# Kernel optimization log

Measured on AMD Instinct MI355X. Metric: run time of the kernel, lower is better.

## Reference

```python
import jax, jax.numpy as jnp
import numpy as np

B, T, N, D = 16, 48, 256, 64
K_HEADS = 8


def setup_inputs() -> dict:
    key = jax.random.key(0)
    ks = jax.random.split(key, 12)
    return {
        "query": jax.random.normal(ks[0], (B, T, N, D), jnp.float32),
        "key": jax.random.normal(ks[1], (B, T, N, D), jnp.float32),
        "value": jax.random.normal(ks[2], (B, T, N, D), jnp.float32),
        "key_w": jax.random.normal(ks[3], (B, T, D, D), jnp.float32) * 0.05,
        "key_b": jax.random.normal(ks[4], (B, T, D), jnp.float32) * 0.05,
        "value_w": jax.random.normal(ks[5], (B, T, D, D), jnp.float32) * 0.05,
        "value_b": jax.random.normal(ks[6], (B, T, D), jnp.float32) * 0.05,
        "proj1_w": jax.random.normal(ks[7], (D, D), jnp.float32) * 0.05,
        "proj1_b": jax.random.normal(ks[8], (D,), jnp.float32) * 0.05,
        "proj2_w": jax.random.normal(ks[9], (D, D), jnp.float32) * 0.05,
        "proj2_b": jax.random.normal(ks[10], (D,), jnp.float32) * 0.05,
        "rate": jnp.full((1,), 0.8, jnp.float32),
    }


def reference(query, key, value, key_w, key_b, value_w, value_b,
              proj1_w, proj1_b, proj2_w, proj2_b, rate):
    b, t, n, d = query.shape
    hs = d // K_HEADS
    # per-(batch,time) projections (LinearCustom)
    k = jnp.einsum('btnd,btde->btne', key, key_w) + key_b[:, :, None, :]
    v = jnp.einsum('btnd,btde->btne', value, value_w) + value_b[:, :, None, :]
    # split heads along channel dim (matches torch.split on dim -1)
    qh = query.reshape(b, t, n, K_HEADS, hs)
    kh = k.reshape(b, t, n, K_HEADS, hs)
    vh = v.reshape(b, t, n, K_HEADS, hs)
    # scores: [b, h, n, q, k]
    scores = jnp.einsum('bqnhd,bknhd->bhnqk', qh, kh) / jnp.sqrt(jnp.asarray(hs, query.dtype))
    # time decay: b_time_decays[..., i, j] = (T-1-i) + 1 = T - i (depends on query pos only)
    dec = (t - jnp.arange(t, dtype=scores.dtype))[:, None]  # [T, 1], broadcasts over key axis
    s = jax.nn.sigmoid(scores)
    denom = 1.0 + jax.nn.sigmoid(s * jax.nn.sigmoid(rate) * dec)
    att = jax.nn.softmax(jnp.tanh(s / denom), axis=-1)
    x = jnp.einsum('bhnqk,bknhd->bqnhd', att, vh).reshape(b, t, n, d)
    x = jnp.tanh(x @ proj1_w.T + proj1_b)
    return x @ proj2_w.T + proj2_b
```

## Files before the change

### kernel.cpp

```cpp
#include <hip/hip_runtime.h>


#define B_ 16
#define T_ 48
#define N_ 256
#define D_ 64

__device__ __forceinline__ float rcpf(float x) { return __builtin_amdgcn_rcpf(x); }
__device__ __forceinline__ float ex2(float x) { return __builtin_amdgcn_exp2f(x); }
#define LOG2E 1.4426950408889634f

__global__ __launch_bounds__(256) void proj_kv_kernel(
    const float* __restrict__ key, const float* __restrict__ key_w, const float* __restrict__ key_b,
    const float* __restrict__ value, const float* __restrict__ value_w, const float* __restrict__ value_b,
    float* __restrict__ k_out, float* __restrict__ v_out)
{
    const int bt = blockIdx.x;
    const int which = blockIdx.y;
    const float* __restrict__ in = (which ? value : key) + (size_t)bt * N_ * D_;
    const float* __restrict__ w  = (which ? value_w : key_w) + (size_t)bt * D_ * D_;
    const float* __restrict__ bb = (which ? value_b : key_b) + (size_t)bt * D_;
    float* __restrict__ out = (which ? v_out : k_out) + (size_t)bt * N_ * D_;

    __shared__ float Wl[D_][D_];
    __shared__ float Xl[128][68];
    __shared__ float Bl[D_];

    const int tid = threadIdx.x;
    #pragma unroll
    for (int i = tid; i < D_ * D_; i += 256) Wl[i >> 6][i & 63] = w[i];
    if (tid < D_) Bl[tid] = bb[tid];

    const int cg = tid & 7;
    const int rg = tid >> 3;

    for (int n0 = 0; n0 < N_; n0 += 128) {
        __syncthreads();
        #pragma unroll
        for (int i = tid; i < 128 * D_ / 4; i += 256) {
            const int e = i * 4;
            *(float4*)&Xl[e >> 6][e & 63] = *(const float4*)&in[(size_t)n0 * D_ + e];
        }
        __syncthreads();

        float acc[4][8];
        #pragma unroll
        for (int j = 0; j < 4; ++j)
            #pragma unroll
            for (int i = 0; i < 8; ++i) acc[j][i] = Bl[cg * 8 + i];

        #pragma unroll 8
        for (int d = 0; d < D_; ++d) {
            const float4 w0 = *(const float4*)&Wl[d][cg * 8];
            const float4 w1 = *(const float4*)&Wl[d][cg * 8 + 4];
            #pragma unroll
            for (int j = 0; j < 4; ++j) {
                const float a = Xl[rg + 32 * j][d];
                acc[j][0] += a * w0.x; acc[j][1] += a * w0.y;
                acc[j][2] += a * w0.z; acc[j][3] += a * w0.w;
                acc[j][4] += a * w1.x; acc[j][5] += a * w1.y;
                acc[j][6] += a * w1.z; acc[j][7] += a * w1.w;
            }
        }

        #pragma unroll
        for (int j = 0; j < 4; ++j) {
            const size_t row = (size_t)(n0 + rg + 32 * j);
            *(float4*)&out[row * D_ + cg * 8]     = make_float4(acc[j][0], acc[j][1], acc[j][2], acc[j][3]);
            *(float4*)&out[row * D_ + cg * 8 + 4] = make_float4(acc[j][4], acc[j][5], acc[j][6], acc[j][7]);
        }
    }
}

__global__ __launch_bounds__(256) void attn_kernel(
    const float* __restrict__ query, float* __restrict__ k_xatt, const float* __restrict__ v_in,
    const float* __restrict__ rate)
{
    const int b  = blockIdx.x >> 7;
    const int n0 = (blockIdx.x & 127) * 2;

    __shared__ float K[2][T_][68];
    __shared__ float V[2][T_][68];

    const int tid = threadIdx.x;
    #pragma unroll
    for (int i = tid; i < T_ * 16; i += 256) {
        const int t = i >> 4, d4 = (i & 15) * 4;
        const size_t g0 = ((size_t)(b * T_ + t) * N_ + n0) * D_ + d4;
        *(float4*)&K[0][t][d4] = *(const float4*)&k_xatt[g0];
        *(float4*)&V[0][t][d4] = *(const float4*)&v_in[g0];
        *(float4*)&K[1][t][d4] = *(const float4*)&k_xatt[g0 + D_];
        *(float4*)&V[1][t][d4] = *(const float4*)&v_in[g0 + D_];
    }
    const float rsig = rcpf(1.0f + ex2(-rate[0] * LOG2E));

    const int nl = tid >> 7;
    const int r  = tid & 127;
    const int qg = r >> 3;
    const int h  = r & 7;
    const int n  = n0 + nl;

    const float C1 = 0.35355339059327373f * LOG2E;
    float4 qa[3], qb[3];
    float rdn[3];
    #pragma unroll
    for (int j = 0; j < 3; ++j) {
        const int q = qg + 16 * j;
        const size_t g = ((size_t)(b * T_ + q) * N_ + n) * D_ + h * 8;
        const float4 a = *(const float4*)&query[g];
        const float4 c = *(const float4*)&query[g + 4];
        qa[j] = make_float4(-C1 * a.x, -C1 * a.y, -C1 * a.z, -C1 * a.w);
        qb[j] = make_float4(-C1 * c.x, -C1 * c.y, -C1 * c.z, -C1 * c.w);
        rdn[j] = -rsig * (float)(T_ - q) * LOG2E;
    }
    __syncthreads();

    float4 acc0[3], acc1[3];
    float ssum[3];
    #pragma unroll
    for (int j = 0; j < 3; ++j) {
        acc0[j] = make_float4(0.f, 0.f, 0.f, 0.f);
        acc1[j] = make_float4(0.f, 0.f, 0.f, 0.f);
        ssum[j] = 0.f;
    }

    #pragma unroll 2
    for (int tk = 0; tk < T_; ++tk) {
        const float4 ka = *(const float4*)&K[nl][tk][h * 8];
        const float4 kb = *(const float4*)&K[nl][tk][h * 8 + 4];
        const float4 va = *(const float4*)&V[nl][tk][h * 8];
        const float4 vb = *(const float4*)&V[nl][tk][h * 8 + 4];
        #pragma unroll
        for (int j = 0; j < 3; ++j) {
            const float dn = qa[j].x * ka.x + qa[j].y * ka.y + qa[j].z * ka.z + qa[j].w * ka.w
                           + qb[j].x * kb.x + qb[j].y * kb.y + qb[j].z * kb.z + qb[j].w * kb.w;
            const float s   = rcpf(1.0f + ex2(dn));
            const float s2  = rcpf(1.0f + ex2(s * rdn[j]));
            const float arg = s * rcpf(1.0f + s2);
            const float x2  = arg * arg;
            const float th  = arg * (15.0f + x2) * rcpf(15.0f + 6.0f * x2);
            const float e   = ex2(th * LOG2E);
            ssum[j] += e;
            acc0[j].x += e * va.x; acc0[j].y += e * va.y; acc0[j].z += e * va.z; acc0[j].w += e * va.w;
            acc1[j].x += e * vb.x; acc1[j].y += e * vb.y; acc1[j].z += e * vb.z; acc1[j].w += e * vb.w;
        }
    }

    #pragma unroll
    for (int j = 0; j < 3; ++j) {
        const float inv = rcpf(ssum[j]);
        const int q = qg + 16 * j;
        const size_t g = ((size_t)(b * T_ + q) * N_ + n) * D_ + h * 8;
        *(float4*)&k_xatt[g]     = make_float4(acc0[j].x * inv, acc0[j].y * inv, acc0[j].z * inv, acc0[j].w * inv);
        *(float4*)&k_xatt[g + 4] = make_float4(acc1[j].x * inv, acc1[j].y * inv, acc1[j].z * inv, acc1[j].w * inv);
    }
}

__global__ __launch_bounds__(256) void wtrans_kernel(
    const float* __restrict__ p1w, const float* __restrict__ p2w,
    float* __restrict__ w1t, float* __restrict__ w2t)
{
    const int i = blockIdx.x * 256 + threadIdx.x;
    if (i < D_ * D_) {
        const int d = i >> 6, c = i & 63;
        w1t[i] = p1w[c * 64 + d];
        w2t[i] = p2w[c * 64 + d];
    }
}

__global__ __launch_bounds__(256) void out_proj_kernel(
    const float* __restrict__ xatt,
    const float* __restrict__ w1t, const float* __restrict__ p1b,
    const float* __restrict__ w2t, const float* __restrict__ p2b,
    float* __restrict__ out)
{
    __shared__ float Xt[D_][132];

    const int tid = threadIdx.x;
    const size_t m0 = (size_t)blockIdx.x * 128;

    #pragma unroll
    for (int i = tid; i < 128 * 16; i += 256) {
        const int row = i >> 4, d4 = (i & 15) * 4;
        const float4 xv = *(const float4*)&xatt[(m0 + row) * D_ + d4];
        Xt[d4 + 0][row] = xv.x;
        Xt[d4 + 1][row] = xv.y;
        Xt[d4 + 2][row] = xv.z;
        Xt[d4 + 3][row] = xv.w;
    }
    __syncthreads();

    const int l  = tid & 63;
    const int c0 = __builtin_amdgcn_readfirstlane((tid >> 6) * 16);

    float a0[16], a1[16];
    #pragma unroll
    for (int c = 0; c < 16; ++c) {
        const float bv = p1b[c0 + c];
        a0[c] = bv; a1[c] = bv;
    }
    for (int d = 0; d < D_; ++d) {
        const float x0 = Xt[d][l];
        const float x1 = Xt[d][l + 64];
        const float* wr = w1t + __builtin_amdgcn_readfirstlane(d * 64 + c0);
        #pragma unroll
        for (int c = 0; c < 16; ++c) {
            const float wv = wr[c];
            a0[c] += x0 * wv;
            a1[c] += x1 * wv;
        }
    }
    #pragma unroll
    for (int c = 0; c < 16; ++c) {
        a0[c] = 1.0f - 2.0f * rcpf(ex2(a0[c] * (2.0f * LOG2E)) + 1.0f);
        a1[c] = 1.0f - 2.0f * rcpf(ex2(a1[c] * (2.0f * LOG2E)) + 1.0f);
    }
    __syncthreads();
    #pragma unroll
    for (int c = 0; c < 16; ++c) {
        Xt[c0 + c][l]      = a0[c];
        Xt[c0 + c][l + 64] = a1[c];
    }
    __syncthreads();

    float o0[16], o1[16];
    #pragma unroll
    for (int c = 0; c < 16; ++c) {
        const float bv = p2b[c0 + c];
        o0[c] = bv; o1[c] = bv;
    }
    for (int d = 0; d < D_; ++d) {
        const float x0 = Xt[d][l];
        const float x1 = Xt[d][l + 64];
        const float* wr = w2t + __builtin_amdgcn_readfirstlane(d * 64 + c0);
        #pragma unroll
        for (int c = 0; c < 16; ++c) {
            const float wv = wr[c];
            o0[c] += x0 * wv;
            o1[c] += x1 * wv;
        }
    }
    #pragma unroll
    for (int k = 0; k < 4; ++k) {
        *(float4*)&out[(m0 + l) * D_ + c0 + 4 * k]      = make_float4(o0[4*k], o0[4*k+1], o0[4*k+2], o0[4*k+3]);
        *(float4*)&out[(m0 + l + 64) * D_ + c0 + 4 * k] = make_float4(o1[4*k], o1[4*k+1], o1[4*k+2], o1[4*k+3]);
    }
}

extern "C" void kernel_launch(void* const* d_in, const int* in_sizes, int n_in,
                              void* d_out, int out_size, void* d_ws, size_t ws_size,
                              hipStream_t stream) {
    const float* query   = (const float*)d_in[0];
    const float* key     = (const float*)d_in[1];
    const float* value   = (const float*)d_in[2];
    const float* key_w   = (const float*)d_in[3];
    const float* key_b   = (const float*)d_in[4];
    const float* value_w = (const float*)d_in[5];
    const float* value_b = (const float*)d_in[6];
    const float* p1w     = (const float*)d_in[7];
    const float* p1b     = (const float*)d_in[8];
    const float* p2w     = (const float*)d_in[9];
    const float* p2b     = (const float*)d_in[10];
    const float* rate    = (const float*)d_in[11];
    float* out = (float*)d_out;

    float* kws = (float*)d_ws;
    float* vws = kws + (size_t)B_ * T_ * N_ * D_;
    float* w1t = vws;
    float* w2t = vws + D_ * D_;

    dim3 gridA(B_ * T_, 2);
    proj_kv_kernel<<<gridA, 256, 0, stream>>>(key, key_w, key_b, value, value_w, value_b, kws, vws);
    attn_kernel<<<B_ * (N_ / 2), 256, 0, stream>>>(query, kws, vws, rate);
    wtrans_kernel<<<16, 256, 0, stream>>>(p1w, p2w, w1t, w2t);
    out_proj_kernel<<<(B_ * T_ * N_) / 128, 256, 0, stream>>>(kws, w1t, p1b, w2t, p2b, out);
}
```

Measured before the change: 241.6 us.

## Fuse output projections into attention kernel and simplify nested sigmoid math

The two output projections (linear, tanh, linear) now run inside the attention kernel on the attention result staged in shared memory, reusing the K/V LDS buffers. This removes the global write and re-read of the attention output, plus the weight-transpose and out-projection launches. Weights are read straight from global memory as float4 rows, with no transposed copy. The inner loop also merges two reciprocals of the nested sigmoid into one and raises the unroll factor, at the cost of more register pressure and uncoalesced weight loads per thread.

```diff
diff --git a/kernel.cpp b/kernel.cpp
--- a/kernel.cpp
+++ b/kernel.cpp
@@ -72,9 +72,11 @@
     }
 }
 
-__global__ __launch_bounds__(256) void attn_kernel(
-    const float* __restrict__ query, float* __restrict__ k_xatt, const float* __restrict__ v_in,
-    const float* __restrict__ rate)
+__global__ __launch_bounds__(256) void attn_fused_kernel(
+    const float* __restrict__ query, const float* __restrict__ k_in, const float* __restrict__ v_in,
+    const float* __restrict__ p1w, const float* __restrict__ p1b,
+    const float* __restrict__ p2w, const float* __restrict__ p2b,
+    const float* __restrict__ rate, float* __restrict__ out)
 {
     const int b  = blockIdx.x >> 7;
     const int n0 = (blockIdx.x & 127) * 2;
@@ -87,9 +89,9 @@
     for (int i = tid; i < T_ * 16; i += 256) {
         const int t = i >> 4, d4 = (i & 15) * 4;
         const size_t g0 = ((size_t)(b * T_ + t) * N_ + n0) * D_ + d4;
-        *(float4*)&K[0][t][d4] = *(const float4*)&k_xatt[g0];
+        *(float4*)&K[0][t][d4] = *(const float4*)&k_in[g0];
         *(float4*)&V[0][t][d4] = *(const float4*)&v_in[g0];
-        *(float4*)&K[1][t][d4] = *(const float4*)&k_xatt[g0 + D_];
+        *(float4*)&K[1][t][d4] = *(const float4*)&k_in[g0 + D_];
         *(float4*)&V[1][t][d4] = *(const float4*)&v_in[g0 + D_];
     }
     const float rsig = rcpf(1.0f + ex2(-rate[0] * LOG2E));
@@ -124,7 +126,7 @@
         ssum[j] = 0.f;
     }
 
-    #pragma unroll 2
+    #pragma unroll 4
     for (int tk = 0; tk < T_; ++tk) {
         const float4 ka = *(const float4*)&K[nl][tk][h * 8];
         const float4 kb = *(const float4*)&K[nl][tk][h * 8 + 4];
@@ -134,9 +136,10 @@
         for (int j = 0; j < 3; ++j) {
             const float dn = qa[j].x * ka.x + qa[j].y * ka.y + qa[j].z * ka.z + qa[j].w * ka.w
                            + qb[j].x * kb.x + qb[j].y * kb.y + qb[j].z * kb.z + qb[j].w * kb.w;
-            const float s   = rcpf(1.0f + ex2(dn));
-            const float s2  = rcpf(1.0f + ex2(s * rdn[j]));
-            const float arg = s * rcpf(1.0f + s2);
+            const float E1  = ex2(dn);
+            const float s   = rcpf(1.0f + E1);
+            const float E2  = ex2(s * rdn[j]);
+            const float arg = s * (1.0f + E2) * rcpf(2.0f + E2);
             const float x2  = arg * arg;
             const float th  = arg * (15.0f + x2) * rcpf(15.0f + 6.0f * x2);
             const float e   = ex2(th * LOG2E);
@@ -146,104 +149,80 @@
         }
     }
 
+    __syncthreads();
     #pragma unroll
     for (int j = 0; j < 3; ++j) {
         const float inv = rcpf(ssum[j]);
         const int q = qg + 16 * j;
-        const size_t g = ((size_t)(b * T_ + q) * N_ + n) * D_ + h * 8;
-        *(float4*)&k_xatt[g]     = make_float4(acc0[j].x * inv, acc0[j].y * inv, acc0[j].z * inv, acc0[j].w * inv);
-        *(float4*)&k_xatt[g + 4] = make_float4(acc1[j].x * inv, acc1[j].y * inv, acc1[j].z * inv, acc1[j].w * inv);
-    }
-}
-
-__global__ __launch_bounds__(256) void wtrans_kernel(
-    const float* __restrict__ p1w, const float* __restrict__ p2w,
-    float* __restrict__ w1t, float* __restrict__ w2t)
-{
-    const int i = blockIdx.x * 256 + threadIdx.x;
-    if (i < D_ * D_) {
-        const int d = i >> 6, c = i & 63;
-        w1t[i] = p1w[c * 64 + d];
-        w2t[i] = p2w[c * 64 + d];
-    }
-}
-
-__global__ __launch_bounds__(256) void out_proj_kernel(
-    const float* __restrict__ xatt,
-    const float* __restrict__ w1t, const float* __restrict__ p1b,
-    const float* __restrict__ w2t, const float* __restrict__ p2b,
-    float* __restrict__ out)
-{
-    __shared__ float Xt[D_][132];
-
-    const int tid = threadIdx.x;
-    const size_t m0 = (size_t)blockIdx.x * 128;
-
-    #pragma unroll
-    for (int i = tid; i < 128 * 16; i += 256) {
-        const int row = i >> 4, d4 = (i & 15) * 4;
-        const float4 xv = *(const float4*)&xatt[(m0 + row) * D_ + d4];
-        Xt[d4 + 0][row] = xv.x;
-        Xt[d4 + 1][row] = xv.y;
-        Xt[d4 + 2][row] = xv.z;
-        Xt[d4 + 3][row] = xv.w;
-    }
-    __syncthreads();
-
-    const int l  = tid & 63;
-    const int c0 = __builtin_amdgcn_readfirstlane((tid >> 6) * 16);
-
-    float a0[16], a1[16];
-    #pragma unroll
-    for (int c = 0; c < 16; ++c) {
-        const float bv = p1b[c0 + c];
-        a0[c] = bv; a1[c] = bv;
-    }
-    for (int d = 0; d < D_; ++d) {
-        const float x0 = Xt[d][l];
-        const float x1 = Xt[d][l + 64];
-        const float* wr = w1t + __builtin_amdgcn_readfirstlane(d * 64 + c0);
-        #pragma unroll
-        for (int c = 0; c < 16; ++c) {
-            const float wv = wr[c];
-            a0[c] += x0 * wv;
-            a1[c] += x1 * wv;
-        }
-    }
-    #pragma unroll
-    for (int c = 0; c < 16; ++c) {
-        a0[c] = 1.0f - 2.0f * rcpf(ex2(a0[c] * (2.0f * LOG2E)) + 1.0f);
-        a1[c] = 1.0f - 2.0f * rcpf(ex2(a1[c] * (2.0f * LOG2E)) + 1.0f);
-    }
-    __syncthreads();
-    #pragma unroll
-    for (int c = 0; c < 16; ++c) {
-        Xt[c0 + c][l]      = a0[c];
-        Xt[c0 + c][l + 64] = a1[c];
-    }
-    __syncthreads();
-
-    float o0[16], o1[16];
-    #pragma unroll
-    for (int c = 0; c < 16; ++c) {
-        const float bv = p2b[c0 + c];
-        o0[c] = bv; o1[c] = bv;
-    }
-    for (int d = 0; d < D_; ++d) {
-        const float x0 = Xt[d][l];
-        const float x1 = Xt[d][l + 64];
-        const float* wr = w2t + __builtin_amdgcn_readfirstlane(d * 64 + c0);
-        #pragma unroll
-        for (int c = 0; c < 16; ++c) {
-            const float wv = wr[c];
-            o0[c] += x0 * wv;
-            o1[c] += x1 * wv;
-        }
-    }
-    #pragma unroll
-    for (int k = 0; k < 4; ++k) {
-        *(float4*)&out[(m0 + l) * D_ + c0 + 4 * k]      = make_float4(o0[4*k], o0[4*k+1], o0[4*k+2], o0[4*k+3]);
-        *(float4*)&out[(m0 + l + 64) * D_ + c0 + 4 * k] = make_float4(o1[4*k], o1[4*k+1], o1[4*k+2], o1[4*k+3]);
+        *(float4*)&K[nl][q][h * 8]     = make_float4(acc0[j].x * inv, acc0[j].y * inv, acc0[j].z * inv, acc0[j].w * inv);
+        *(float4*)&K[nl][q][h * 8 + 4] = make_float4(acc1[j].x * inv, acc1[j].y * inv, acc1[j].z * inv, acc1[j].w * inv);
+    }
+    __syncthreads();
+
+    {
+        float a[3][8];
+        const float4 b0 = *(const float4*)&p1b[h * 8];
+        const float4 b1 = *(const float4*)&p1b[h * 8 + 4];
+        #pragma unroll
+        for (int j = 0; j < 3; ++j) {
+            a[j][0] = b0.x; a[j][1] = b0.y; a[j][2] = b0.z; a[j][3] = b0.w;
+            a[j][4] = b1.x; a[j][5] = b1.y; a[j][6] = b1.z; a[j][7] = b1.w;
+        }
+        #pragma unroll 2
+        for (int d0 = 0; d0 < D_; d0 += 4) {
+            float4 xv[3];
+            #pragma unroll
+            for (int j = 0; j < 3; ++j) xv[j] = *(const float4*)&K[nl][qg + 16 * j][d0];
+            #pragma unroll
+            for (int c = 0; c < 8; ++c) {
+                const float4 wc = *(const float4*)&p1w[(h * 8 + c) * D_ + d0];
+                #pragma unroll
+                for (int j = 0; j < 3; ++j)
+                    a[j][c] += xv[j].x * wc.x + xv[j].y * wc.y + xv[j].z * wc.z + xv[j].w * wc.w;
+            }
+        }
+        #pragma unroll
+        for (int j = 0; j < 3; ++j) {
+            const int q = qg + 16 * j;
+            float t[8];
+            #pragma unroll
+            for (int c = 0; c < 8; ++c)
+                t[c] = 1.0f - 2.0f * rcpf(ex2(a[j][c] * (2.0f * LOG2E)) + 1.0f);
+            *(float4*)&V[nl][q][h * 8]     = make_float4(t[0], t[1], t[2], t[3]);
+            *(float4*)&V[nl][q][h * 8 + 4] = make_float4(t[4], t[5], t[6], t[7]);
+        }
+    }
+    __syncthreads();
+
+    {
+        float a[3][8];
+        const float4 b0 = *(const float4*)&p2b[h * 8];
+        const float4 b1 = *(const float4*)&p2b[h * 8 + 4];
+        #pragma unroll
+        for (int j = 0; j < 3; ++j) {
+            a[j][0] = b0.x; a[j][1] = b0.y; a[j][2] = b0.z; a[j][3] = b0.w;
+            a[j][4] = b1.x; a[j][5] = b1.y; a[j][6] = b1.z; a[j][7] = b1.w;
+        }
+        #pragma unroll 2
+        for (int d0 = 0; d0 < D_; d0 += 4) {
+            float4 xv[3];
+            #pragma unroll
+            for (int j = 0; j < 3; ++j) xv[j] = *(const float4*)&V[nl][qg + 16 * j][d0];
+            #pragma unroll
+            for (int c = 0; c < 8; ++c) {
+                const float4 wc = *(const float4*)&p2w[(h * 8 + c) * D_ + d0];
+                #pragma unroll
+                for (int j = 0; j < 3; ++j)
+                    a[j][c] += xv[j].x * wc.x + xv[j].y * wc.y + xv[j].z * wc.z + xv[j].w * wc.w;
+            }
+        }
+        #pragma unroll
+        for (int j = 0; j < 3; ++j) {
+            const int q = qg + 16 * j;
+            const size_t og = ((size_t)(b * T_ + q) * N_ + n) * D_ + h * 8;
+            *(float4*)&out[og]     = make_float4(a[j][0], a[j][1], a[j][2], a[j][3]);
+            *(float4*)&out[og + 4] = make_float4(a[j][4], a[j][5], a[j][6], a[j][7]);
+        }
     }
 }
 
@@ -266,12 +245,8 @@
 
     float* kws = (float*)d_ws;
     float* vws = kws + (size_t)B_ * T_ * N_ * D_;
-    float* w1t = vws;
-    float* w2t = vws + D_ * D_;
 
     dim3 gridA(B_ * T_, 2);
     proj_kv_kernel<<<gridA, 256, 0, stream>>>(key, key_w, key_b, value, value_w, value_b, kws, vws);
-    attn_kernel<<<B_ * (N_ / 2), 256, 0, stream>>>(query, kws, vws, rate);
-    wtrans_kernel<<<16, 256, 0, stream>>>(p1w, p2w, w1t, w2t);
-    out_proj_kernel<<<(B_ * T_ * N_) / 128, 256, 0, stream>>>(kws, w1t, p1b, w2t, p2b, out);
+    attn_fused_kernel<<<B_ * (N_ / 2), 256, 0, stream>>>(query, kws, vws, p1w, p1b, p2w, p2b, rate, out);
 }
```

Measured after the change: 337.2 us. +39.6%, slower.
